# Optimization experiments

Hardware: AMD Instinct MI355X
Metric: run time of the kernel (lower is better)

The kernel has to match this reference:

```python
import jax, jax.numpy as jnp
import numpy as np

B, T, HID = 1, 8192, 2048
NH, NKV, D = 32, 8, 64
BLK, LOCAL, GLOB = 64, 8, 1
THETA = 10000.0
SCALE = 1.0 / float(np.sqrt(D))
NEG = -1e9


def _sparse_tables(nb):
    """Replicates HumanVAttention._get_sparse_tables: per query block i select
    global blocks [0, GLOB) then local blocks [i-LOCAL+1, i], dedup keeping order."""
    max_sel = LOCAL + GLOB
    idx = np.zeros((nb, max_sel), np.int32)
    valid = np.zeros((nb, max_sel), bool)
    for i in range(nb):
        sel = [g for g in range(GLOB) if g < nb]
        sel += list(range(max(0, i - (LOCAL - 1)), i + 1))
        li, seen = [], set()
        for x in sel:
            if x not in seen:
                li.append(x); seen.add(x)
        idx[i, :len(li)] = li
        valid[i, :len(li)] = True
    return idx, valid


def _rotate_half(x):
    x1, x2 = x[..., : x.shape[-1] // 2], x[..., x.shape[-1] // 2:]
    return jnp.concatenate((-x2, x1), axis=-1)


def setup_inputs() -> dict:
    key = jax.random.key(0)
    ks = jax.random.split(key, 5)
    s = 0.02
    return {
        "hidden_states": jax.random.normal(ks[0], (B, T, HID), jnp.float32),
        "Wq": jax.random.normal(ks[1], (NH * D, HID), jnp.float32) * s,
        "Wk": jax.random.normal(ks[2], (NKV * D, HID), jnp.float32) * s,
        "Wv": jax.random.normal(ks[3], (NKV * D, HID), jnp.float32) * s,
        "Wo": jax.random.normal(ks[4], (NH * D, NH * D), jnp.float32) * s,
    }


def reference(hidden_states, Wq, Wk, Wv, Wo):
    hs = hidden_states
    # projections (nn.Linear: y = x @ W.T)
    q = (hs @ Wq.T).reshape(B, T, NH, D).transpose(0, 2, 1, 3)     # [B,NH,T,D]
    k = (hs @ Wk.T).reshape(B, T, NKV, D).transpose(0, 2, 1, 3)    # [B,NKV,T,D]
    v = (hs @ Wv.T).reshape(B, T, NKV, D).transpose(0, 2, 1, 3)

    # RoPE (full rotary factor)
    inv = 1.0 / (THETA ** (jnp.arange(0, D, 2, dtype=jnp.float32) / D))
    fr = jnp.arange(T, dtype=jnp.float32)[:, None] * inv[None, :]  # [T,D/2]
    emb = jnp.concatenate([fr, fr], axis=-1)                       # [T,D]
    cos = jnp.cos(emb)[None, None]                                 # [1,1,T,D]
    sin = jnp.sin(emb)[None, None]
    q = q * cos + _rotate_half(q) * sin
    k = k * cos + _rotate_half(k) * sin

    nb = T // BLK
    G = NH // NKV
    idx_np, valid_np = _sparse_tables(nb)
    max_sel = idx_np.shape[1]

    # gather selected K/V blocks per query block
    kb = k.reshape(B, NKV, nb, BLK, D)
    vb = v.reshape(B, NKV, nb, BLK, D)
    idx = jnp.asarray(idx_np)
    k_sel = kb[:, :, idx].reshape(B, NKV, nb, max_sel * BLK, D)    # [B,NKV,nb,M,D]
    v_sel = vb[:, :, idx].reshape(B, NKV, nb, max_sel * BLK, D)

    qg = q.reshape(B, NKV, G, nb, BLK, D)                          # grouped queries
    scores = jnp.einsum('bkgnqd,bknmd->bkgnqm',
                        qg.astype(jnp.float32), k_sel.astype(jnp.float32)) * SCALE

    # causal + validity mask over selected keys (static, built in numpy)
    kpos = (idx_np[:, :, None] * BLK + np.arange(BLK)).reshape(nb, -1)   # [nb,M]
    qpos = np.arange(nb)[:, None] * BLK + np.arange(BLK)                 # [nb,BLK]
    valid_flat = np.repeat(valid_np, BLK, axis=1)                        # [nb,M]
    allowed = valid_flat[:, None, :] & (kpos[:, None, :] <= qpos[:, :, None])
    scores = jnp.where(jnp.asarray(allowed)[None, None, None], scores, NEG)

    probs = jax.nn.softmax(scores, axis=-1)
    out = jnp.einsum('bkgnqm,bknmd->bkgnqd', probs.astype(v.dtype), v_sel)
    out = out.astype(hs.dtype).reshape(B, NH, T, D).transpose(0, 2, 1, 3)
    out = out.reshape(B, T, NH * D)
    return out @ Wo.T
```

## Files before the change

kernel.cpp:

```cpp
#include <hip/hip_runtime.h>
#include <cstdint>
#include <cstddef>

typedef __bf16 bf16;
typedef __attribute__((ext_vector_type(8))) __bf16 bf16x8;
typedef __attribute__((ext_vector_type(4))) __bf16 bf16x4;
typedef __attribute__((ext_vector_type(4))) float f32x4;

#define ATT_SCALE 0.125f

__device__ __forceinline__ f32x4 mfma16(bf16x8 a, bf16x8 b, f32x4 c) {
  return __builtin_amdgcn_mfma_f32_16x16x32_bf16(a, b, c, 0, 0, 0);
}

__device__ __forceinline__ void gload16(const bf16* g, bf16* l) {
  __builtin_amdgcn_global_load_lds((__attribute__((address_space(1))) void*)g,
                                   (__attribute__((address_space(3))) void*)l,
                                   16, 0, 0);
}

__global__ __launch_bounds__(256) void prep_all(const float* __restrict__ hs,
                                                const float* __restrict__ Wq,
                                                const float* __restrict__ Wk,
                                                const float* __restrict__ Wv,
                                                const float* __restrict__ Wo,
                                                bf16* __restrict__ hs16, bf16* __restrict__ wq16,
                                                bf16* __restrict__ wk16, bf16* __restrict__ wv16,
                                                bf16* __restrict__ wo16,
                                                float* __restrict__ cosT, float* __restrict__ sinT) {
  int b = blockIdx.x, t = threadIdx.x;
  const float* src; bf16* dst; int i;
  if (b < 16384)      { src = hs; dst = hs16; i = b * 256 + t; }
  else if (b < 20480) { src = Wq; dst = wq16; i = (b - 16384) * 256 + t; }
  else if (b < 21504) { src = Wk; dst = wk16; i = (b - 20480) * 256 + t; }
  else if (b < 22528) { src = Wv; dst = wv16; i = (b - 21504) * 256 + t; }
  else if (b < 26624) { src = Wo; dst = wo16; i = (b - 22528) * 256 + t; }
  else {
    int idx = (b - 26624) * 256 + t;
    int tt = idx >> 5, j = idx & 31;
    float inv = exp2f(-(float)j * (13.287712379549449f / 32.0f));
    float fr = (float)tt * inv;
    cosT[idx] = cosf(fr); sinT[idx] = sinf(fr);
    return;
  }
  float4 v = *((const float4*)src + i);
  bf16x4 o;
  o[0] = (bf16)v.x; o[1] = (bf16)v.y; o[2] = (bf16)v.z; o[3] = (bf16)v.w;
  *((bf16x4*)dst + i) = o;
}

__global__ __launch_bounds__(512) void gemm_qkv(const bf16* __restrict__ A,
                                                const bf16* __restrict__ B0,
                                                const bf16* __restrict__ B1,
                                                const bf16* __restrict__ B2,
                                                bf16* __restrict__ C,
                                                const float* __restrict__ cosT,
                                                const float* __restrict__ sinT) {
  __shared__ bf16 As[3][8192];
  __shared__ bf16 Bs[3][12288];
  const int tid = threadIdx.x, lane = tid & 63, wid = tid >> 6;
  const int m0 = blockIdx.x * 256, n0 = blockIdx.y * 384;
  const int wr = wid >> 1, wc = wid & 1;
  const int fr = lane & 15, g4 = lane >> 4;
  const int sw8 = (g4 ^ ((fr >> 1) & 3)) * 8;

  f32x4 acc[4][12] = {};

  auto brow = [&](int n) -> const bf16* {
    if (n < 2048) return B0 + (size_t)n * 2048;
    if (n < 2560) return B1 + (size_t)(n - 2048) * 2048;
    return B2 + (size_t)(n - 2560) * 2048;
  };

  const int ra0 = tid >> 2, ra1 = 128 + (tid >> 2), rb2r = 256 + (tid >> 2);
  const bf16* aS0 = A + (size_t)(m0 + ra0) * 2048 + ((tid & 3) ^ ((ra0 >> 1) & 3)) * 8;
  const bf16* aS1 = A + (size_t)(m0 + ra1) * 2048 + ((tid & 3) ^ ((ra1 >> 1) & 3)) * 8;
  const bf16* bS0 = brow(n0 + ra0) + ((tid & 3) ^ ((ra0 >> 1) & 3)) * 8;
  const bf16* bS1 = brow(n0 + ra1) + ((tid & 3) ^ ((ra1 >> 1) & 3)) * 8;
  const bf16* bS2 = brow(n0 + rb2r) + ((tid & 3) ^ ((rb2r >> 1) & 3)) * 8;
  const int d0 = wid * 512, d1 = 4096 + wid * 512, d2 = 8192 + wid * 512;

#define STQA(BS, KT)  { bf16* d = &As[BS][0]; \
    gload16(aS0 + (KT) * 32, d + d0); gload16(aS1 + (KT) * 32, d + d1); }
#define STQB0(BS, KT) { bf16* d = &Bs[BS][0]; \
    gload16(bS0 + (KT) * 32, d + d0); gload16(bS1 + (KT) * 32, d + d1); }
#define STQB1(BS, KT) { gload16(bS2 + (KT) * 32, &Bs[BS][0] + d2); }

#define QTILE(KT, BI, BS, VM, STG) { \
    asm volatile("s_waitcnt vmcnt(" VM ")" ::: "memory"); \
    __builtin_amdgcn_s_barrier(); \
    __builtin_amdgcn_sched_barrier(0); \
    const bf16* Ab = &As[BI][0]; \
    const bf16* Bb = &Bs[BI][0]; \
    bf16x8 af[4], bfr[4]; \
    _Pragma("unroll") for (int mf = 0; mf < 4; ++mf) \
      af[mf] = *(const bf16x8*)(Ab + (wr * 64 + mf * 16 + fr) * 32 + sw8); \
    _Pragma("unroll") for (int q = 0; q < 4; ++q) \
      bfr[q] = *(const bf16x8*)(Bb + (wc * 192 + q * 16 + fr) * 32 + sw8); \
    if (STG) STQA(BS, (KT) + 2); \
    __builtin_amdgcn_s_setprio(1); \
    _Pragma("unroll") for (int mf = 0; mf < 4; ++mf) \
      _Pragma("unroll") for (int q = 0; q < 4; ++q) \
        acc[mf][q] = mfma16(af[mf], bfr[q], acc[mf][q]); \
    __builtin_amdgcn_s_setprio(0); \
    _Pragma("unroll") for (int q = 0; q < 4; ++q) \
      bfr[q] = *(const bf16x8*)(Bb + (wc * 192 + 64 + q * 16 + fr) * 32 + sw8); \
    if (STG) STQB0(BS, (KT) + 2); \
    __builtin_amdgcn_s_setprio(1); \
    _Pragma("unroll") for (int mf = 0; mf < 4; ++mf) \
      _Pragma("unroll") for (int q = 0; q < 4; ++q) \
        acc[mf][4 + q] = mfma16(af[mf], bfr[q], acc[mf][4 + q]); \
    __builtin_amdgcn_s_setprio(0); \
    _Pragma("unroll") for (int q = 0; q < 4; ++q) \
      bfr[q] = *(const bf16x8*)(Bb + (wc * 192 + 128 + q * 16 + fr) * 32 + sw8); \
    if (STG) STQB1(BS, (KT) + 2); \
    __builtin_amdgcn_s_setprio(1); \
    _Pragma("unroll") for (int mf = 0; mf < 4; ++mf) \
      _Pragma("unroll") for (int q = 0; q < 4; ++q) \
        acc[mf][8 + q] = mfma16(af[mf], bfr[q], acc[mf][8 + q]); \
    __builtin_amdgcn_s_setprio(0); \
  }

  STQA(0, 0); STQB0(0, 0); STQB1(0, 0);
  STQA(1, 1); STQB0(1, 1); STQB1(1, 1);

  int bi = 0, bs = 2;
  for (int kt = 0; kt < 62; ++kt) {
    QTILE(kt, bi, bs, "5", 1)
    bi = (bi == 2) ? 0 : bi + 1;
    bs = (bs == 2) ? 0 : bs + 1;
  }
  QTILE(62, bi, bs, "5", 0)
  bi = (bi == 2) ? 0 : bi + 1;
  QTILE(63, bi, bi, "0", 0)
#undef QTILE
#undef STQA
#undef STQB0
#undef STQB1

  const int fc = lane & 15, fr4 = (lane >> 4) * 4;
#pragma unroll
  for (int mf = 0; mf < 4; ++mf)
#pragma unroll
    for (int i = 0; i < 4; ++i) {
      size_t row = (size_t)(m0 + wr * 64 + mf * 16 + fr4 + i);
      bf16* base = C + row * 3072 + n0 + wc * 192;
      const float* cr = cosT + row * 32;
      const float* sr = sinT + row * 32;
#pragma unroll
      for (int g = 0; g < 3; ++g) {
        if (n0 + wc * 192 + g * 64 < 2560) {
#pragma unroll
          for (int q = 0; q < 2; ++q) {
            int j = q * 16 + fc;
            float c = cr[j], sn = sr[j];
            float x1 = acc[mf][g * 4 + q][i], x2 = acc[mf][g * 4 + q + 2][i];
            base[g * 64 + j]      = (bf16)(x1 * c - x2 * sn);
            base[g * 64 + j + 32] = (bf16)(x2 * c + x1 * sn);
          }
        } else {
#pragma unroll
          for (int q = 0; q < 4; ++q)
            base[g * 64 + q * 16 + fc] = (bf16)acc[mf][g * 4 + q][i];
        }
      }
    }
}

__global__ __launch_bounds__(512, 2) void gemm_out(const bf16* __restrict__ A,
                                                   const bf16* __restrict__ B0,
                                                   float* __restrict__ Cout) {
  __shared__ bf16 As[4][8192];
  __shared__ bf16 Bs[4][8192];
  const int tid = threadIdx.x, lane = tid & 63, wid = tid >> 6;
  const int m0 = blockIdx.x * 256, n0 = blockIdx.y * 256;
  const int wr = wid >> 2, wc = wid & 3;
  const int fr = lane & 15, g4 = lane >> 4;
  const int sw8 = (g4 ^ ((fr >> 1) & 3)) * 8;
  const int K = 2048, N = 2048;

  f32x4 acc[8][4] = {};

  const bf16* aS0; const bf16* aS1; const bf16* bS0; const bf16* bS1;
  {
    int c0 = tid, r0 = c0 >> 2, l0 = (c0 & 3) ^ ((r0 >> 1) & 3);
    int c1 = 512 + tid, r1 = c1 >> 2, l1 = (c1 & 3) ^ ((r1 >> 1) & 3);
    aS0 = A + (size_t)(m0 + r0) * K + l0 * 8;
    aS1 = A + (size_t)(m0 + r1) * K + l1 * 8;
    bS0 = B0 + (size_t)(n0 + r0) * K + l0 * 8;
    bS1 = B0 + (size_t)(n0 + r1) * K + l1 * 8;
  }
  const int dst0 = wid * 512;
  const int dst1 = 4096 + wid * 512;

#define STAGE_A(KT) { bf16* d = &As[(KT) & 3][0]; \
    gload16(aS0 + (KT) * 32, d + dst0); gload16(aS1 + (KT) * 32, d + dst1); }
#define STAGE_B(KT) { bf16* d = &Bs[(KT) & 3][0]; \
    gload16(bS0 + (KT) * 32, d + dst0); gload16(bS1 + (KT) * 32, d + dst1); }

#define KTILE(KT, VM, STG) { \
    asm volatile("s_waitcnt vmcnt(" VM ")" ::: "memory"); \
    __builtin_amdgcn_s_barrier(); \
    __builtin_amdgcn_sched_barrier(0); \
    const bf16* Ab = &As[(KT) & 3][0]; \
    const bf16* Bb = &Bs[(KT) & 3][0]; \
    bf16x8 bfr[4], af[4]; \
    _Pragma("unroll") for (int nf = 0; nf < 4; ++nf) \
      bfr[nf] = *(const bf16x8*)(Bb + (wc * 64 + nf * 16 + fr) * 32 + sw8); \
    _Pragma("unroll") for (int mf = 0; mf < 4; ++mf) \
      af[mf] = *(const bf16x8*)(Ab + (wr * 128 + mf * 16 + fr) * 32 + sw8); \
    if (STG) STAGE_A((KT) + 3); \
    __builtin_amdgcn_s_setprio(1); \
    _Pragma("unroll") for (int mf = 0; mf < 4; ++mf) \
      _Pragma("unroll") for (int nf = 0; nf < 4; ++nf) \
        acc[mf][nf] = mfma16(af[mf], bfr[nf], acc[mf][nf]); \
    __builtin_amdgcn_s_setprio(0); \
    _Pragma("unroll") for (int mf = 0; mf < 4; ++mf) \
      af[mf] = *(const bf16x8*)(Ab + (wr * 128 + 64 + mf * 16 + fr) * 32 + sw8); \
    if (STG) STAGE_B((KT) + 3); \
    __builtin_amdgcn_s_setprio(1); \
    _Pragma("unroll") for (int mf = 0; mf < 4; ++mf) \
      _Pragma("unroll") for (int nf = 0; nf < 4; ++nf) \
        acc[4 + mf][nf] = mfma16(af[mf], bfr[nf], acc[4 + mf][nf]); \
    __builtin_amdgcn_s_setprio(0); \
  }

  STAGE_A(0); STAGE_B(0);
  STAGE_A(1); STAGE_B(1);
  STAGE_A(2); STAGE_B(2);

  const int NT = K >> 5;
  for (int kt = 0; kt < NT - 3; ++kt) KTILE(kt, "8", 1)
  KTILE(NT - 3, "8", 0)
  KTILE(NT - 2, "4", 0)
  KTILE(NT - 1, "0", 0)
#undef KTILE
#undef STAGE_A
#undef STAGE_B

  const int fc = lane & 15, fr4 = (lane >> 4) * 4;
#pragma unroll
  for (int am = 0; am < 8; ++am)
#pragma unroll
    for (int i = 0; i < 4; ++i) {
      size_t row = (size_t)(m0 + wr * 128 + am * 16 + fr4 + i);
#pragma unroll
      for (int nf = 0; nf < 4; ++nf) {
        int col = n0 + wc * 64 + nf * 16 + fc;
        Cout[row * (size_t)N + col] = acc[am][nf][i];
      }
    }
}

__global__ __launch_bounds__(512) void attn_sparse(const bf16* __restrict__ qkv,
                                                   bf16* __restrict__ attn) {
  const int iblk = blockIdx.x;
  const int kv = blockIdx.y >> 1, pr = blockIdx.y & 1;
  const int tid = threadIdx.x, lane = tid & 63, wid = tid >> 6;
  const int h = kv * 4 + pr * 2 + (wid >> 2);
  const int rg = wid & 3;

  __shared__ bf16 Ks[2][64 * 64];
  __shared__ bf16 Vt[2][64 * 72];

  const int qcol = h * 64, kcol = 2048 + kv * 64, vcol = 2560 + kv * 64;
  const size_t trow0 = (size_t)iblk * 64;
  const int fr = lane & 15, g4 = lane >> 4, fk = g4 * 8, fr4 = g4 * 4;

  const bf16* qrow = qkv + (trow0 + rg * 16 + fr) * 3072 + qcol;
  bf16x8 bq0 = *(const bf16x8*)(qrow + fk);
  bf16x8 bq1 = *(const bf16x8*)(qrow + 32 + fk);

  float mrun = -INFINITY, lrun = 0.f;
  f32x4 acc[4] = {};

  const int kr = tid >> 3, ks = tid & 7;
  const int pik = ((kr >> 5) << 5) + (((kr & 15) >> 2) << 3) + (((kr >> 4) & 1) << 2) + (kr & 3);
  const int kso = ((ks ^ (kr & 7)) * 8);
  const int vp = tid & 31, vd0 = (tid >> 5) * 4;

  const int kb0m = fk, kb1m = fk + 4, kb2m = fk + 32, kb3m = fk + 36;

  const int nsel = (iblk < 8) ? (iblk + 1) : 9;
  auto jof = [&](int js) { return (iblk < 8) ? js : ((js == 0) ? 0 : iblk - 8 + js); };

  {
    const size_t krow = (size_t)jof(0) * 64;
    gload16(qkv + (krow + pik) * 3072 + kcol + kso, &Ks[0][0] + (tid >> 6) * 512);
    const bf16* v0p = qkv + (krow + 2 * vp) * 3072 + vcol + vd0;
    uint64_t a = *(const uint64_t*)v0p;
    uint64_t b = *(const uint64_t*)(v0p + 3072);
#pragma unroll
    for (int e = 0; e < 4; ++e) {
      uint32_t w = (uint32_t)((a >> (16 * e)) & 0xFFFF) |
                   ((uint32_t)((b >> (16 * e)) & 0xFFFF) << 16);
      *(uint32_t*)(&Vt[0][0] + (vd0 + e) * 72 + 2 * vp) = w;
    }
  }
  __syncthreads();

  for (int js = 0; js < nsel; ++js) {
    const int cur = js & 1;
    const int jblk = jof(js);
    const bool pre = (js + 1 < nsel);
    const size_t nrow = pre ? (size_t)jof(js + 1) * 64 : 0;

    uint64_t va = 0, vb2 = 0;
    if (pre) {
      const bf16* v0p = qkv + (nrow + 2 * vp) * 3072 + vcol + vd0;
      va = *(const uint64_t*)v0p;
      vb2 = *(const uint64_t*)(v0p + 3072);
    }

    f32x4 s[4];
    __builtin_amdgcn_s_setprio(1);
#pragma unroll
    for (int n = 0; n < 4; ++n) {
      const char* krowp = (const char*)&Ks[cur][0] + (n * 16 + fr) * 128;
      bf16x8 ka = *(const bf16x8*)(krowp + ((g4 ^ (fr & 7)) << 4));
      bf16x8 kc = *(const bf16x8*)(krowp + (((4 + g4) ^ (fr & 7)) << 4));
      f32x4 z = {};
      z = mfma16(ka, bq0, z);
      s[n] = mfma16(kc, bq1, z);
    }
    __builtin_amdgcn_s_setprio(0);

    if (pre)
      gload16(qkv + (nrow + pik) * 3072 + kcol + kso, &Ks[cur ^ 1][0] + (tid >> 6) * 512);

    if (jblk == iblk) {
      const int qr = rg * 16 + fr;
#pragma unroll
      for (int i = 0; i < 4; ++i) {
        if (kb0m + i > qr) s[0][i] = -1e30f;
        if (kb1m + i > qr) s[1][i] = -1e30f;
        if (kb2m + i > qr) s[2][i] = -1e30f;
        if (kb3m + i > qr) s[3][i] = -1e30f;
      }
    }

    float t0 = fmaxf(fmaxf(s[0][0], s[0][1]), fmaxf(s[0][2], s[0][3]));
    float t1 = fmaxf(fmaxf(s[1][0], s[1][1]), fmaxf(s[1][2], s[1][3]));
    float t2 = fmaxf(fmaxf(s[2][0], s[2][1]), fmaxf(s[2][2], s[2][3]));
    float t3 = fmaxf(fmaxf(s[3][0], s[3][1]), fmaxf(s[3][2], s[3][3]));
    float mx = fmaxf(fmaxf(t0, t1), fmaxf(t2, t3));
    mx = fmaxf(mx, __shfl_xor(mx, 16, 64));
    mx = fmaxf(mx, __shfl_xor(mx, 32, 64));
    float mnew = fmaxf(mrun, mx);
    float corr = __expf((mrun - mnew) * ATT_SCALE);
    mrun = mnew;
    const float msc = mnew * ATT_SCALE;
    float ps = 0.f;
#pragma unroll
    for (int n = 0; n < 4; ++n) {
      float p0 = __expf(fmaf(s[n][0], ATT_SCALE, -msc));
      float p1 = __expf(fmaf(s[n][1], ATT_SCALE, -msc));
      float p2 = __expf(fmaf(s[n][2], ATT_SCALE, -msc));
      float p3 = __expf(fmaf(s[n][3], ATT_SCALE, -msc));
      s[n][0] = p0; s[n][1] = p1; s[n][2] = p2; s[n][3] = p3;
      ps += (p0 + p1) + (p2 + p3);
    }
    ps += __shfl_xor(ps, 16, 64);
    ps += __shfl_xor(ps, 32, 64);
    lrun = lrun * corr + ps;

    float cq[4];
#pragma unroll
    for (int i = 0; i < 4; ++i) cq[i] = __shfl(corr, fr4 + i, 64);
#pragma unroll
    for (int n = 0; n < 4; ++n)
#pragma unroll
      for (int i = 0; i < 4; ++i) acc[n][i] *= cq[i];

    bf16x8 pa0, pa1;
#pragma unroll
    for (int i = 0; i < 4; ++i) {
      pa0[i]     = (bf16)s[0][i];
      pa0[4 + i] = (bf16)s[1][i];
      pa1[i]     = (bf16)s[2][i];
      pa1[4 + i] = (bf16)s[3][i];
    }

    if (pre) {
#pragma unroll
      for (int e = 0; e < 4; ++e) {
        uint32_t w = (uint32_t)((va >> (16 * e)) & 0xFFFF) |
                     ((uint32_t)((vb2 >> (16 * e)) & 0xFFFF) << 16);
        *(uint32_t*)(&Vt[cur ^ 1][0] + (vd0 + e) * 72 + 2 * vp) = w;
      }
    }

    __builtin_amdgcn_s_setprio(1);
#pragma unroll
    for (int n = 0; n < 4; ++n) {
      bf16x8 vb0 = *(const bf16x8*)(&Vt[cur][0] + (n * 16 + fr) * 72 + fk);
      bf16x8 vb1 = *(const bf16x8*)(&Vt[cur][0] + (n * 16 + fr) * 72 + 32 + fk);
      acc[n] = mfma16(pa0, vb0, acc[n]);
      acc[n] = mfma16(pa1, vb1, acc[n]);
    }
    __builtin_amdgcn_s_setprio(0);

    __syncthreads();
  }

  float lq[4];
#pragma unroll
  for (int i = 0; i < 4; ++i) lq[i] = __shfl(lrun, fr4 + i, 64);
#pragma unroll
  for (int i = 0; i < 4; ++i) {
    float rl = 1.0f / lq[i];
    size_t t = trow0 + rg * 16 + fr4 + i;
#pragma unroll
    for (int n = 0; n < 4; ++n)
      attn[t * 2048 + h * 64 + n * 16 + fr] = (bf16)(acc[n][i] * rl);
  }
}

extern "C" void kernel_launch(void* const* d_in, const int* in_sizes, int n_in,
                              void* d_out, int out_size, void* d_ws, size_t ws_size,
                              hipStream_t stream) {
  (void)in_sizes; (void)n_in; (void)out_size; (void)ws_size;
  const float* hs = (const float*)d_in[0];
  const float* Wq = (const float*)d_in[1];
  const float* Wk = (const float*)d_in[2];
  const float* Wv = (const float*)d_in[3];
  const float* Wo = (const float*)d_in[4];
  float* out = (float*)d_out;

  char* ws = (char*)d_ws;
  bf16* hs16 = (bf16*)(ws + 0);
  bf16* qkv  = (bf16*)(ws + 33554432);
  bf16* attn = (bf16*)(ws + 83886080);
  bf16* wq16 = (bf16*)(ws + 117440512);
  bf16* wk16 = (bf16*)(ws + 125829120);
  bf16* wv16 = (bf16*)(ws + 127926272);
  bf16* wo16 = (bf16*)(ws + 130023424);
  float* cosT = (float*)(ws + 138412032);
  float* sinT = (float*)(ws + 139460608);

  prep_all<<<27648, 256, 0, stream>>>(hs, Wq, Wk, Wv, Wo,
                                      hs16, wq16, wk16, wv16, wo16, cosT, sinT);

  gemm_qkv<<<dim3(32, 8), 512, 0, stream>>>(hs16, wq16, wk16, wv16, qkv, cosT, sinT);
  attn_sparse<<<dim3(128, 16), 512, 0, stream>>>(qkv, attn);
  gemm_out<<<dim3(32, 8), 512, 0, stream>>>(attn, wo16, out);
}
```

Before: 267.6 us.

## Process all four GQA heads per block with two query tiles per wave

The attention kernel now covers all four query heads of a KV group in one workgroup instead of splitting them across two. Each wave handles 32 query rows as two 16-row tiles, so every K/V fragment read from LDS is reused twice, and the grid is halved. This cuts redundant K/V global loads and LDS staging per head. In exchange each wave needs more registers, and with half as many workgroups there is less parallelism across CUs.

```diff
diff --git a/kernel.cpp b/kernel.cpp
--- a/kernel.cpp
+++ b/kernel.cpp
@@ -255,10 +255,10 @@
 __global__ __launch_bounds__(512) void attn_sparse(const bf16* __restrict__ qkv,
                                                    bf16* __restrict__ attn) {
   const int iblk = blockIdx.x;
-  const int kv = blockIdx.y >> 1, pr = blockIdx.y & 1;
+  const int kv = blockIdx.y;
   const int tid = threadIdx.x, lane = tid & 63, wid = tid >> 6;
-  const int h = kv * 4 + pr * 2 + (wid >> 2);
-  const int rg = wid & 3;
+  const int h = kv * 4 + (wid >> 1);
+  const int rh = wid & 1;
 
   __shared__ bf16 Ks[2][64 * 64];
   __shared__ bf16 Vt[2][64 * 72];
@@ -267,12 +267,15 @@
   const size_t trow0 = (size_t)iblk * 64;
   const int fr = lane & 15, g4 = lane >> 4, fk = g4 * 8, fr4 = g4 * 4;
 
-  const bf16* qrow = qkv + (trow0 + rg * 16 + fr) * 3072 + qcol;
-  bf16x8 bq0 = *(const bf16x8*)(qrow + fk);
-  bf16x8 bq1 = *(const bf16x8*)(qrow + 32 + fk);
-
-  float mrun = -INFINITY, lrun = 0.f;
-  f32x4 acc[4] = {};
+  const bf16* qr0 = qkv + (trow0 + rh * 32 + fr) * 3072 + qcol;
+  const bf16* qr1 = qkv + (trow0 + rh * 32 + 16 + fr) * 3072 + qcol;
+  bf16x8 bqA0 = *(const bf16x8*)(qr0 + fk);
+  bf16x8 bqA1 = *(const bf16x8*)(qr0 + 32 + fk);
+  bf16x8 bqB0 = *(const bf16x8*)(qr1 + fk);
+  bf16x8 bqB1 = *(const bf16x8*)(qr1 + 32 + fk);
+
+  float mA = -INFINITY, lA = 0.f, mB = -INFINITY, lB = 0.f;
+  f32x4 accA[4] = {}, accB[4] = {};
 
   const int kr = tid >> 3, ks = tid & 7;
   const int pik = ((kr >> 5) << 5) + (((kr & 15) >> 2) << 3) + (((kr >> 4) & 1) << 2) + (kr & 3);
@@ -312,16 +315,18 @@
       vb2 = *(const uint64_t*)(v0p + 3072);
     }
 
-    f32x4 s[4];
+    f32x4 sA[4], sB[4];
     __builtin_amdgcn_s_setprio(1);
 #pragma unroll
     for (int n = 0; n < 4; ++n) {
       const char* krowp = (const char*)&Ks[cur][0] + (n * 16 + fr) * 128;
       bf16x8 ka = *(const bf16x8*)(krowp + ((g4 ^ (fr & 7)) << 4));
       bf16x8 kc = *(const bf16x8*)(krowp + (((4 + g4) ^ (fr & 7)) << 4));
-      f32x4 z = {};
-      z = mfma16(ka, bq0, z);
-      s[n] = mfma16(kc, bq1, z);
+      f32x4 zA = {}, zB = {};
+      zA = mfma16(ka, bqA0, zA);
+      sA[n] = mfma16(kc, bqA1, zA);
+      zB = mfma16(ka, bqB0, zB);
+      sB[n] = mfma16(kc, bqB1, zB);
     }
     __builtin_amdgcn_s_setprio(0);
 
@@ -329,56 +334,98 @@
       gload16(qkv + (nrow + pik) * 3072 + kcol + kso, &Ks[cur ^ 1][0] + (tid >> 6) * 512);
 
     if (jblk == iblk) {
-      const int qr = rg * 16 + fr;
+      const int qrA = rh * 32 + fr, qrB = qrA + 16;
 #pragma unroll
       for (int i = 0; i < 4; ++i) {
-        if (kb0m + i > qr) s[0][i] = -1e30f;
-        if (kb1m + i > qr) s[1][i] = -1e30f;
-        if (kb2m + i > qr) s[2][i] = -1e30f;
-        if (kb3m + i > qr) s[3][i] = -1e30f;
+        if (kb0m + i > qrA) sA[0][i] = -1e30f;
+        if (kb1m + i > qrA) sA[1][i] = -1e30f;
+        if (kb2m + i > qrA) sA[2][i] = -1e30f;
+        if (kb3m + i > qrA) sA[3][i] = -1e30f;
+        if (kb0m + i > qrB) sB[0][i] = -1e30f;
+        if (kb1m + i > qrB) sB[1][i] = -1e30f;
+        if (kb2m + i > qrB) sB[2][i] = -1e30f;
+        if (kb3m + i > qrB) sB[3][i] = -1e30f;
       }
     }
 
-    float t0 = fmaxf(fmaxf(s[0][0], s[0][1]), fmaxf(s[0][2], s[0][3]));
-    float t1 = fmaxf(fmaxf(s[1][0], s[1][1]), fmaxf(s[1][2], s[1][3]));
-    float t2 = fmaxf(fmaxf(s[2][0], s[2][1]), fmaxf(s[2][2], s[2][3]));
-    float t3 = fmaxf(fmaxf(s[3][0], s[3][1]), fmaxf(s[3][2], s[3][3]));
-    float mx = fmaxf(fmaxf(t0, t1), fmaxf(t2, t3));
-    mx = fmaxf(mx, __shfl_xor(mx, 16, 64));
-    mx = fmaxf(mx, __shfl_xor(mx, 32, 64));
-    float mnew = fmaxf(mrun, mx);
-    float corr = __expf((mrun - mnew) * ATT_SCALE);
-    mrun = mnew;
-    const float msc = mnew * ATT_SCALE;
-    float ps = 0.f;
-#pragma unroll
-    for (int n = 0; n < 4; ++n) {
-      float p0 = __expf(fmaf(s[n][0], ATT_SCALE, -msc));
-      float p1 = __expf(fmaf(s[n][1], ATT_SCALE, -msc));
-      float p2 = __expf(fmaf(s[n][2], ATT_SCALE, -msc));
-      float p3 = __expf(fmaf(s[n][3], ATT_SCALE, -msc));
-      s[n][0] = p0; s[n][1] = p1; s[n][2] = p2; s[n][3] = p3;
-      ps += (p0 + p1) + (p2 + p3);
-    }
-    ps += __shfl_xor(ps, 16, 64);
-    ps += __shfl_xor(ps, 32, 64);
-    lrun = lrun * corr + ps;
-
-    float cq[4];
-#pragma unroll
-    for (int i = 0; i < 4; ++i) cq[i] = __shfl(corr, fr4 + i, 64);
-#pragma unroll
-    for (int n = 0; n < 4; ++n)
-#pragma unroll
-      for (int i = 0; i < 4; ++i) acc[n][i] *= cq[i];
-
-    bf16x8 pa0, pa1;
+    {
+      float t0 = fmaxf(fmaxf(sA[0][0], sA[0][1]), fmaxf(sA[0][2], sA[0][3]));
+      float t1 = fmaxf(fmaxf(sA[1][0], sA[1][1]), fmaxf(sA[1][2], sA[1][3]));
+      float t2 = fmaxf(fmaxf(sA[2][0], sA[2][1]), fmaxf(sA[2][2], sA[2][3]));
+      float t3 = fmaxf(fmaxf(sA[3][0], sA[3][1]), fmaxf(sA[3][2], sA[3][3]));
+      float mx = fmaxf(fmaxf(t0, t1), fmaxf(t2, t3));
+      mx = fmaxf(mx, __shfl_xor(mx, 16, 64));
+      mx = fmaxf(mx, __shfl_xor(mx, 32, 64));
+      float mnew = fmaxf(mA, mx);
+      float corr = __expf((mA - mnew) * ATT_SCALE);
+      mA = mnew;
+      const float msc = mnew * ATT_SCALE;
+      float ps = 0.f;
+#pragma unroll
+      for (int n = 0; n < 4; ++n) {
+        float p0 = __expf(fmaf(sA[n][0], ATT_SCALE, -msc));
+        float p1 = __expf(fmaf(sA[n][1], ATT_SCALE, -msc));
+        float p2 = __expf(fmaf(sA[n][2], ATT_SCALE, -msc));
+        float p3 = __expf(fmaf(sA[n][3], ATT_SCALE, -msc));
+        sA[n][0] = p0; sA[n][1] = p1; sA[n][2] = p2; sA[n][3] = p3;
+        ps += (p0 + p1) + (p2 + p3);
+      }
+      ps += __shfl_xor(ps, 16, 64);
+      ps += __shfl_xor(ps, 32, 64);
+      lA = lA * corr + ps;
+      float cq[4];
+#pragma unroll
+      for (int i = 0; i < 4; ++i) cq[i] = __shfl(corr, fr4 + i, 64);
+#pragma unroll
+      for (int n = 0; n < 4; ++n)
+#pragma unroll
+        for (int i = 0; i < 4; ++i) accA[n][i] *= cq[i];
+    }
+    {
+      float t0 = fmaxf(fmaxf(sB[0][0], sB[0][1]), fmaxf(sB[0][2], sB[0][3]));
+      float t1 = fmaxf(fmaxf(sB[1][0], sB[1][1]), fmaxf(sB[1][2], sB[1][3]));
+      float t2 = fmaxf(fmaxf(sB[2][0], sB[2][1]), fmaxf(sB[2][2], sB[2][3]));
+      float t3 = fmaxf(fmaxf(sB[3][0], sB[3][1]), fmaxf(sB[3][2], sB[3][3]));
+      float mx = fmaxf(fmaxf(t0, t1), fmaxf(t2, t3));
+      mx = fmaxf(mx, __shfl_xor(mx, 16, 64));
+      mx = fmaxf(mx, __shfl_xor(mx, 32, 64));
+      float mnew = fmaxf(mB, mx);
+      float corr = __expf((mB - mnew) * ATT_SCALE);
+      mB = mnew;
+      const float msc = mnew * ATT_SCALE;
+      float ps = 0.f;
+#pragma unroll
+      for (int n = 0; n < 4; ++n) {
+        float p0 = __expf(fmaf(sB[n][0], ATT_SCALE, -msc));
+        float p1 = __expf(fmaf(sB[n][1], ATT_SCALE, -msc));
+        float p2 = __expf(fmaf(sB[n][2], ATT_SCALE, -msc));
+        float p3 = __expf(fmaf(sB[n][3], ATT_SCALE, -msc));
+        sB[n][0] = p0; sB[n][1] = p1; sB[n][2] = p2; sB[n][3] = p3;
+        ps += (p0 + p1) + (p2 + p3);
+      }
+      ps += __shfl_xor(ps, 16, 64);
+      ps += __shfl_xor(ps, 32, 64);
+      lB = lB * corr + ps;
+      float cq[4];
+#pragma unroll
+      for (int i = 0; i < 4; ++i) cq[i] = __shfl(corr, fr4 + i, 64);
+#pragma unroll
+      for (int n = 0; n < 4; ++n)
+#pragma unroll
+        for (int i = 0; i < 4; ++i) accB[n][i] *= cq[i];
+    }
+
+    bf16x8 paA0, paA1, paB0, paB1;
 #pragma unroll
     for (int i = 0; i < 4; ++i) {
-      pa0[i]     = (bf16)s[0][i];
-      pa0[4 + i] = (bf16)s[1][i];
-      pa1[i]     = (bf16)s[2][i];
-      pa1[4 + i] = (bf16)s[3][i];
+      paA0[i]     = (bf16)sA[0][i];
+      paA0[4 + i] = (bf16)sA[1][i];
+      paA1[i]     = (bf16)sA[2][i];
+      paA1[4 + i] = (bf16)sA[3][i];
+      paB0[i]     = (bf16)sB[0][i];
+      paB0[4 + i] = (bf16)sB[1][i];
+      paB1[i]     = (bf16)sB[2][i];
+      paB1[4 + i] = (bf16)sB[3][i];
     }
 
     if (pre) {
@@ -395,24 +442,32 @@
     for (int n = 0; n < 4; ++n) {
       bf16x8 vb0 = *(const bf16x8*)(&Vt[cur][0] + (n * 16 + fr) * 72 + fk);
       bf16x8 vb1 = *(const bf16x8*)(&Vt[cur][0] + (n * 16 + fr) * 72 + 32 + fk);
-      acc[n] = mfma16(pa0, vb0, acc[n]);
-      acc[n] = mfma16(pa1, vb1, acc[n]);
+      accA[n] = mfma16(paA0, vb0, accA[n]);
+      accA[n] = mfma16(paA1, vb1, accA[n]);
+      accB[n] = mfma16(paB0, vb0, accB[n]);
+      accB[n] = mfma16(paB1, vb1, accB[n]);
     }
     __builtin_amdgcn_s_setprio(0);
 
     __syncthreads();
   }
 
-  float lq[4];
-#pragma unroll
-  for (int i = 0; i < 4; ++i) lq[i] = __shfl(lrun, fr4 + i, 64);
+  float lqA[4], lqB[4];
 #pragma unroll
   for (int i = 0; i < 4; ++i) {
-    float rl = 1.0f / lq[i];
-    size_t t = trow0 + rg * 16 + fr4 + i;
-#pragma unroll
-    for (int n = 0; n < 4; ++n)
-      attn[t * 2048 + h * 64 + n * 16 + fr] = (bf16)(acc[n][i] * rl);
+    lqA[i] = __shfl(lA, fr4 + i, 64);
+    lqB[i] = __shfl(lB, fr4 + i, 64);
+  }
+#pragma unroll
+  for (int i = 0; i < 4; ++i) {
+    float rlA = 1.0f / lqA[i], rlB = 1.0f / lqB[i];
+    size_t tA = trow0 + rh * 32 + fr4 + i;
+    size_t tB = tA + 16;
+#pragma unroll
+    for (int n = 0; n < 4; ++n) {
+      attn[tA * 2048 + h * 64 + n * 16 + fr] = (bf16)(accA[n][i] * rlA);
+      attn[tB * 2048 + h * 64 + n * 16 + fr] = (bf16)(accB[n][i] * rlB);
+    }
   }
 }
 
@@ -442,6 +497,6 @@
                                       hs16, wq16, wk16, wv16, wo16, cosT, sinT);
 
   gemm_qkv<<<dim3(32, 8), 512, 0, stream>>>(hs16, wq16, wk16, wv16, qkv, cosT, sinT);
-  attn_sparse<<<dim3(128, 16), 512, 0, stream>>>(qkv, attn);
+  attn_sparse<<<dim3(128, 8), 512, 0, stream>>>(qkv, attn);
   gemm_out<<<dim3(32, 8), 512, 0, stream>>>(attn, wo16, out);
 }
```

New measurement: 274.4 us. 2.5% more time.
